# Kernel optimization log

Hardware: AMD Instinct MI355X
Metric: run time of the kernel (lower is better)

## Reference

```python
import jax, jax.numpy as jnp
import numpy as np

N = 102400   # total nodes
F = 400      # node features
E = 1638400  # edges
H = 64       # hidden channels
L = 3        # num_layers (hidden convs); +1 final conv to width 1
K = 300      # sort-pool k
NPER = 400   # nodes per graph (uniform graphs)
B = N // NPER
D = H * L + 1  # total_latent_dim = 193


def setup_inputs() -> dict:
    key = jax.random.key(0)
    ks = jax.random.split(key, 20)
    def lin(k, i, o):
        return jax.random.normal(k, (i, o), jnp.float32) / np.sqrt(i)
    inp = {
        "x": jax.random.normal(ks[0], (N, F), jnp.float32),
        "edge_index": jax.random.randint(ks[1], (2, E), 0, N, jnp.int64),
        "W1": lin(ks[2], F, H), "b1": jnp.zeros((H,), jnp.float32),
        "W2": lin(ks[3], H, H), "b2": jnp.zeros((H,), jnp.float32),
        "W3": lin(ks[4], H, H), "b3": jnp.zeros((H,), jnp.float32),
        "W4": lin(ks[5], H, 1), "b4": jnp.zeros((1,), jnp.float32),
        "cw1": jax.random.normal(ks[6], (16, 1, D), jnp.float32) / np.sqrt(D),
        "cb1": jnp.zeros((16,), jnp.float32),
        "cw2": jax.random.normal(ks[7], (32, 16, 5), jnp.float32) / np.sqrt(16 * 5),
        "cb2": jnp.zeros((32,), jnp.float32),
        "mw1": lin(ks[8], 4672, 32), "mb1": jnp.zeros((32,), jnp.float32),
        "mw2": lin(ks[9], 32, 2), "mb2": jnp.zeros((2,), jnp.float32),
    }
    return inp


def _gcn(x, W, b, src, dst, norm):
    h = x @ W                                   # [N, out]
    msg = h[src] * norm[:, None]                # [E', out]
    out = jax.ops.segment_sum(msg, dst, num_segments=N)
    return out + b


def reference(x, edge_index, W1, b1, W2, b2, W3, b3, W4, b4,
              cw1, cb1, cw2, cb2, mw1, mb1, mw2, mb2):
    # GCN normalization with self-loops (D^-1/2 (A+I) D^-1/2)
    loops = jnp.arange(N, dtype=edge_index.dtype)
    src = jnp.concatenate([edge_index[0], loops])
    dst = jnp.concatenate([edge_index[1], loops])
    deg = jax.ops.segment_sum(jnp.ones_like(src, jnp.float32), dst, num_segments=N)
    dis = jax.lax.rsqrt(jnp.maximum(deg, 1.0))
    norm = dis[src] * dis[dst]

    h1 = jnp.tanh(_gcn(x, W1, b1, src, dst, norm))
    h2 = jnp.tanh(_gcn(h1, W2, b2, src, dst, norm))
    h3 = jnp.tanh(_gcn(h2, W3, b3, src, dst, norm))
    h4 = jnp.tanh(_gcn(h3, W4, b4, src, dst, norm))
    feat = jnp.concatenate([h1, h2, h3, h4], axis=-1)  # [N, D]

    # SortAggregation: per-graph sort by last channel (descending), take top-k
    fg = feat.reshape(B, NPER, D)
    order = jnp.argsort(-fg[:, :, -1], axis=1)[:, :K]  # [B, K]
    pooled = jnp.take_along_axis(fg, order[:, :, None], axis=1)  # [B, K, D]
    z = pooled.reshape(B, 1, K * D)

    dn = ("NCH", "OIH", "NCH")
    z = jax.lax.conv_general_dilated(z, cw1, (D,), "VALID", dimension_numbers=dn)
    z = jax.nn.relu(z + cb1[None, :, None])            # [B, 16, K]
    z = jax.lax.reduce_window(z, -jnp.inf, jax.lax.max, (1, 1, 2), (1, 1, 2), "VALID")
    z = jax.lax.conv_general_dilated(z, cw2, (1,), "VALID", dimension_numbers=dn)
    z = jax.nn.relu(z + cb2[None, :, None])            # [B, 32, 146]
    z = z.reshape(B, -1)                               # [B, 4672]
    z = jax.nn.relu(z @ mw1 + mb1)
    return z @ mw2 + mb2                               # [B, 2]
```

## Files before the change

### kernel.cpp

```cpp
#include <hip/hip_runtime.h>
#include <cstdint>
#include <cstddef>

#define Nn 102400
#define Ff 400
#define Ee 1638400
#define Kk 300
#define Bb 256
#define CAP 64

__device__ __forceinline__ float xla_tanhf(float x) {
    const float c = 7.90531110763549805f;
    float xc = fminf(fmaxf(x, -c), c);
    float x2 = __fmul_rn(xc, xc);
    float p = -2.76076847742355e-16f;
    p = __fadd_rn(__fmul_rn(p, x2),  2.00018790482477e-13f);
    p = __fadd_rn(__fmul_rn(p, x2), -8.60467152213735e-11f);
    p = __fadd_rn(__fmul_rn(p, x2),  5.12229709037114e-08f);
    p = __fadd_rn(__fmul_rn(p, x2),  1.48572235717979e-05f);
    p = __fadd_rn(__fmul_rn(p, x2),  6.37261928875436e-04f);
    p = __fadd_rn(__fmul_rn(p, x2),  4.89352455891786e-03f);
    p = __fmul_rn(p, xc);
    float q = 1.19825839466702e-06f;
    q = __fadd_rn(__fmul_rn(q, x2), 1.18534705686654e-04f);
    q = __fadd_rn(__fmul_rn(q, x2), 2.26843463243900e-03f);
    q = __fadd_rn(__fmul_rn(q, x2), 4.89352518554385e-03f);
    float r = __fdiv_rn(p, q);
    return (fabsf(x) < 0.0004f) ? x : r;
}

__global__ void scat_k(const int* __restrict__ ei, int* __restrict__ fill,
                       int* __restrict__ csr) {
    int g = blockIdx.x * 256 + threadIdx.x;
    int2 d2 = *(const int2*)(ei + Ee + 2 * g);
    int e0 = 2 * g, e1 = 2 * g + 1;
    int p0 = atomicAdd(&fill[(size_t)d2.x * 16], 1);
    int p1 = atomicAdd(&fill[(size_t)d2.y * 16], 1);
    if (p0 < CAP) csr[(size_t)d2.x * CAP + p0] = e0;
    if (p1 < CAP) csr[(size_t)d2.y * CAP + p1] = e1;
}

__global__ void dis_k(const int* __restrict__ fill, float* __restrict__ dis,
                      int* __restrict__ degc) {
    int v = blockIdx.x * 256 + threadIdx.x;
    if (v >= Nn) return;
    int d = fill[(size_t)v * 16];
    degc[v] = d;
    dis[v] = 1.0f / sqrtf((float)(d + 1));
}

template <int CH>
__global__ __launch_bounds__(128) void gemm_2w(const float* __restrict__ A,
                                               const float* __restrict__ B,
                                               float* __restrict__ C) {
    constexpr int K = 16 * CH;
    __shared__ __align__(16) float As[16 * 32];
    __shared__ __align__(16) float Bs[16 * 68];
    int tid = threadIdx.x;
    int w = tid >> 6;
    int lane = tid & 63;
    int tx = lane & 15;
    int ty = lane >> 4;
    int base = blockIdx.x * 32;
    int sr = tid >> 2, sq = tid & 3;
    int bk = tid >> 3, bn = (tid & 7) * 8;
    float acc[8][2] = {};
    for (int ch = 0; ch < CH; ++ch) {
        int k0 = ch * 16;
        float4 av = *(const float4*)(A + (size_t)(base + sr) * K + k0 + sq * 4);
        const float* bp = B + (size_t)(k0 + bk) * 64 + bn;
        float4 b0 = *(const float4*)(bp);
        float4 b1 = *(const float4*)(bp + 4);
        __syncthreads();
        As[(sq * 4 + 0) * 32 + sr] = av.x;
        As[(sq * 4 + 1) * 32 + sr] = av.y;
        As[(sq * 4 + 2) * 32 + sr] = av.z;
        As[(sq * 4 + 3) * 32 + sr] = av.w;
        *(float4*)&Bs[bk * 68 + bn]     = b0;
        *(float4*)&Bs[bk * 68 + bn + 4] = b1;
        __syncthreads();
#pragma unroll
        for (int kk = 0; kk < 16; ++kk) {
            float4 f0 = *(const float4*)&As[kk * 32 + ty * 8];
            float4 f1 = *(const float4*)&As[kk * 32 + ty * 8 + 4];
            float2 bb = *(const float2*)&Bs[kk * 68 + w * 32 + tx * 2];
            float av8[8] = {f0.x, f0.y, f0.z, f0.w, f1.x, f1.y, f1.z, f1.w};
#pragma unroll
            for (int r = 0; r < 8; ++r) {
                acc[r][0] = fmaf(av8[r], bb.x, acc[r][0]);
                acc[r][1] = fmaf(av8[r], bb.y, acc[r][1]);
            }
        }
    }
#pragma unroll
    for (int r = 0; r < 8; ++r) {
        float* cp = C + (size_t)(base + ty * 8 + r) * 64 + w * 32 + tx * 2;
        *(float2*)cp = make_float2(acc[r][0], acc[r][1]);
    }
}

template <int CH>
__global__ __launch_bounds__(64) void gemm_w32(const float* __restrict__ A,
                                               const float* __restrict__ B,
                                               float* __restrict__ C) {
    constexpr int K = 16 * CH;
    __shared__ __align__(16) float As[16 * 32];
    __shared__ __align__(16) float Bs[16][68];
    int tid = threadIdx.x;
    int tx = tid & 15;
    int ty = tid >> 4;
    int base = blockIdx.x * 32;
    int sr = tid >> 1, sh = tid & 1;
    int bk = tid >> 2, bn = (tid & 3) * 16;
    float acc[8][4] = {};
    for (int ch = 0; ch < CH; ++ch) {
        int k0 = ch * 16;
        const float* ap = A + (size_t)(base + sr) * K + k0 + sh * 8;
        float4 v0 = *(const float4*)(ap);
        float4 v1 = *(const float4*)(ap + 4);
        float a8[8] = {v0.x, v0.y, v0.z, v0.w, v1.x, v1.y, v1.z, v1.w};
        float4 bv4[4];
        const float* bp = B + (size_t)(k0 + bk) * 64 + bn;
#pragma unroll
        for (int q = 0; q < 4; ++q) bv4[q] = *(const float4*)(bp + q * 4);
        __syncthreads();
#pragma unroll
        for (int q = 0; q < 8; ++q) As[(sh * 8 + q) * 32 + sr] = a8[q];
#pragma unroll
        for (int q = 0; q < 4; ++q) *(float4*)&Bs[bk][bn + q * 4] = bv4[q];
        __syncthreads();
#pragma unroll
        for (int kk = 0; kk < 16; ++kk) {
            float4 f0 = *(const float4*)&As[kk * 32 + ty * 8];
            float4 f1 = *(const float4*)&As[kk * 32 + ty * 8 + 4];
            float av[8] = {f0.x, f0.y, f0.z, f0.w, f1.x, f1.y, f1.z, f1.w};
            float2 b01 = *(const float2*)&Bs[kk][tx * 2];
            float2 b23 = *(const float2*)&Bs[kk][32 + tx * 2];
            float bv[4] = {b01.x, b01.y, b23.x, b23.y};
#pragma unroll
            for (int r = 0; r < 8; ++r)
#pragma unroll
                for (int c = 0; c < 4; ++c) acc[r][c] = fmaf(av[r], bv[c], acc[r][c]);
        }
    }
#pragma unroll
    for (int r = 0; r < 8; ++r) {
        float* cp = C + (size_t)(base + ty * 8 + r) * 64;
        *(float2*)(cp + tx * 2)      = make_float2(acc[r][0], acc[r][1]);
        *(float2*)(cp + 32 + tx * 2) = make_float2(acc[r][2], acc[r][3]);
    }
}

template <int PHASE>
__global__ __launch_bounds__(256, 4) void agg64_k(const float* __restrict__ t,
                                                  const float* __restrict__ bias,
                                                  const float* __restrict__ dis,
                                                  const int* __restrict__ degc,
                                                  const int* __restrict__ ei,
                                                  int* __restrict__ csr,
                                                  float* __restrict__ nrm,
                                                  float* __restrict__ out,
                                                  const float* __restrict__ W4,
                                                  float* __restrict__ t4) {
    __shared__ int   sidx[4][64];
    __shared__ float snr[4][64];
    int lane = threadIdx.x & 63;
    int wv = __builtin_amdgcn_readfirstlane(threadIdx.x >> 6);
    int v = blockIdx.x * 4 + wv;
    int dv = __builtin_amdgcn_readfirstlane(min(degc[v], CAP));
    float dsv = dis[v];
    float tself = t[(size_t)v * 64 + lane];
    float bsl = bias[lane];
    int idxl;
    float nr;
    if (PHASE == 1) {
        int key = (lane < dv) ? csr[(size_t)v * CAP + lane] : 0x7FFFFFFF;
#pragma unroll
        for (int k = 2; k <= 64; k <<= 1) {
#pragma unroll
            for (int j = k >> 1; j; j >>= 1) {
                int other = __shfl_xor(key, j);
                bool up = ((lane & k) == 0);
                bool lower = ((lane & j) == 0);
                key = (lower == up) ? min(key, other) : max(key, other);
            }
        }
        idxl = v;
        if (lane < dv) idxl = ei[key];
        nr = (lane < dv) ? __fmul_rn(dis[idxl], dsv) : 0.0f;
        csr[(size_t)v * CAP + lane] = idxl;
        nrm[(size_t)v * 64 + lane] = nr;
    } else {
        idxl = (lane < dv) ? csr[(size_t)v * CAP + lane] : v;
        nr = nrm[(size_t)v * 64 + lane];
    }
    sidx[wv][lane] = idxl;
    snr[wv][lane] = nr;
    int dvp = (dv + 31) & ~31;
    float acc = 0.0f;
    for (int j = 0; j < dvp; j += 32) {
        float tv[32], nv[32];
#pragma unroll
        for (int q = 0; q < 32; ++q) {
            int u = __builtin_amdgcn_readfirstlane(sidx[wv][j + q]);
            tv[q] = t[(size_t)u * 64 + lane];
        }
#pragma unroll
        for (int q = 0; q < 32; ++q) nv[q] = snr[wv][j + q];
#pragma unroll
        for (int q = 0; q < 32; ++q)
            acc = __fadd_rn(acc, __fmul_rn(tv[q], nv[q]));
    }
    acc = __fadd_rn(acc, __fmul_rn(tself, __fmul_rn(dsv, dsv)));
    float res = xla_tanhf(__fadd_rn(acc, bsl));
    out[(size_t)v * 64 + lane] = res;
    if (W4 != nullptr) {
        float w4l = W4[lane];
        float a4 = 0.0f;
#pragma unroll
        for (int k = 0; k < 64; ++k) {
            float hk = __shfl(res, k);
            float wk = __shfl(w4l, k);
            a4 = fmaf(hk, wk, a4);
        }
        if (lane == 0) t4[v] = a4;
    }
}

__global__ void agg1_k(const float* __restrict__ t4, const float* __restrict__ dis,
                       const int* __restrict__ degc, const int* __restrict__ csr,
                       const float* __restrict__ nrm,
                       const float* __restrict__ b4, float* __restrict__ h4) {
    int v = blockIdx.x * 256 + threadIdx.x;
    if (v >= Nn) return;
    int dv = min(degc[v], CAP);
    float dsv = dis[v];
    const int* row = csr + (size_t)v * CAP;
    const float* nr = nrm + (size_t)v * 64;
    float acc = 0.0f;
    int j = 0;
    for (; j + 16 <= dv; j += 16) {
        int u[16]; float nv[16], tv[16];
#pragma unroll
        for (int q = 0; q < 16; ++q) nv[q] = nr[j + q];
#pragma unroll
        for (int q = 0; q < 16; ++q) u[q] = row[j + q];
#pragma unroll
        for (int q = 0; q < 16; ++q) tv[q] = t4[u[q]];
#pragma unroll
        for (int q = 0; q < 16; ++q)
            acc = __fadd_rn(acc, __fmul_rn(tv[q], nv[q]));
    }
    for (; j + 4 <= dv; j += 4) {
        int u[4]; float nv[4], tv[4];
#pragma unroll
        for (int q = 0; q < 4; ++q) nv[q] = nr[j + q];
#pragma unroll
        for (int q = 0; q < 4; ++q) u[q] = row[j + q];
#pragma unroll
        for (int q = 0; q < 4; ++q) tv[q] = t4[u[q]];
#pragma unroll
        for (int q = 0; q < 4; ++q)
            acc = __fadd_rn(acc, __fmul_rn(tv[q], nv[q]));
    }
    for (; j < dv; ++j)
        acc = __fadd_rn(acc, __fmul_rn(t4[row[j]], nr[j]));
    acc = __fadd_rn(acc, __fmul_rn(t4[v], __fmul_rn(dsv, dsv)));
    h4[v] = xla_tanhf(__fadd_rn(acc, b4[0]));
}

__global__ __launch_bounds__(512) void sort_k(const float* __restrict__ h4,
                                              int* __restrict__ order) {
    __shared__ unsigned int kv[512];
    __shared__ int ki[512];
    int tid = threadIdx.x, g = blockIdx.x;
    unsigned int key = 0xFFFFFFFFu;
    if (tid < 400) {
        unsigned int u = __float_as_uint(h4[g * 400 + tid]);
        u = (u & 0x80000000u) ? ~u : (u | 0x80000000u);
        key = ~u;
    }
    kv[tid] = key; ki[tid] = tid;
    __syncthreads();
    for (int size = 2; size <= 512; size <<= 1) {
        for (int stride = size >> 1; stride > 0; stride >>= 1) {
            int p = tid ^ stride;
            if (p > tid) {
                bool asc = ((tid & size) == 0);
                unsigned int a = kv[tid], b = kv[p];
                int ia = ki[tid], ib = ki[p];
                bool gt = (a > b) || (a == b && ia > ib);
                if (gt == asc) { kv[tid] = b; kv[p] = a; ki[tid] = ib; ki[p] = ia; }
            }
            __syncthreads();
        }
    }
    if (tid < Kk) order[g * Kk + tid] = ki[tid];
}

__global__ __launch_bounds__(128) void conv1_k(const float* __restrict__ h1,
                                               const float* __restrict__ h2,
                                               const float* __restrict__ h3,
                                               const float* __restrict__ h4,
                                               const int* __restrict__ order,
                                               const float* __restrict__ cw1,
                                               const float* __restrict__ cb1,
                                               float* __restrict__ z1) {
    __shared__ double wt[193 * 16];
    int tid = threadIdx.x, b = blockIdx.y;
    for (int i = tid; i < 193 * 16; i += 128) {
        int c = i / 193, d = i % 193;
        wt[d * 16 + c] = (double)cw1[i];
    }
    __syncthreads();
    int kpos = blockIdx.x * 128 + tid;
    if (kpos >= Kk) return;
    int n = b * 400 + order[b * Kk + kpos];
    double acc[16];
#pragma unroll
    for (int c = 0; c < 16; ++c) acc[c] = (double)cb1[c];
    const float* bases[3] = {h1 + (size_t)n * 64, h2 + (size_t)n * 64, h3 + (size_t)n * 64};
    for (int r = 0; r < 3; ++r) {
        const float* p = bases[r];
        for (int d = 0; d < 64; ++d) {
            double xv = (double)p[d];
            const double* wp = &wt[((size_t)r * 64 + d) * 16];
#pragma unroll
            for (int c = 0; c < 16; ++c) acc[c] += xv * wp[c];
        }
    }
    double xl = (double)h4[n];
    {
        const double* wp = &wt[192 * 16];
#pragma unroll
        for (int c = 0; c < 16; ++c) acc[c] += xl * wp[c];
    }
#pragma unroll
    for (int c = 0; c < 16; ++c)
        z1[((size_t)b * 16 + c) * 300 + kpos] = (float)fmax(acc[c], 0.0);
}

__global__ __launch_bounds__(256) void tail_k(const float* __restrict__ z1,
                                              const float* __restrict__ cw2,
                                              const float* __restrict__ cb2,
                                              const float* __restrict__ mw1,
                                              const float* __restrict__ mb1,
                                              const float* __restrict__ mw2,
                                              const float* __restrict__ mb2,
                                              float* __restrict__ out) {
    __shared__ float lz[16 * 150];
    __shared__ float lw[2560];
    __shared__ float lz3[4672];
    __shared__ double red[256];
    __shared__ double s4[32];
    int b = blockIdx.x, tid = threadIdx.x;
    for (int i = tid; i < 2400; i += 256) {
        int bc = i / 150, j = i % 150;
        const float* zp = z1 + ((size_t)b * 16 + bc) * 300 + 2 * j;
        lz[i] = fmaxf(zp[0], zp[1]);
    }
    for (int i = tid; i < 2560; i += 256) lw[i] = cw2[i];
    __syncthreads();
    for (int o = tid; o < 4672; o += 256) {
        int co = o / 146, j = o % 146;
        float acc = cb2[co];
#pragma unroll
        for (int ci = 0; ci < 16; ++ci)
#pragma unroll
            for (int tt = 0; tt < 5; ++tt)
                acc += lz[ci * 150 + j + tt] * lw[co * 80 + ci * 5 + tt];
        lz3[o] = fmaxf(acc, 0.f);
    }
    __syncthreads();
    int o = tid & 31, part = tid >> 5;
    double acc = 0.0;
    for (int i = part * 584; i < (part + 1) * 584; ++i)
        acc += (double)lz3[i] * (double)mw1[(size_t)i * 32 + o];
    red[tid] = acc;
    __syncthreads();
    if (tid < 32) {
        double s = 0.0;
#pragma unroll
        for (int p = 0; p < 8; ++p) s += red[p * 32 + tid];
        s4[tid] = fmax(s + (double)mb1[tid], 0.0);
    }
    __syncthreads();
    if (tid < 2) {
        double s = (double)mb2[tid];
#pragma unroll
        for (int j = 0; j < 32; ++j) s += s4[j] * (double)mw2[j * 2 + tid];
        out[b * 2 + tid] = (float)s;
    }
}

extern "C" void kernel_launch(void* const* d_in, const int* in_sizes, int n_in,
                              void* d_out, int out_size, void* d_ws, size_t ws_size,
                              hipStream_t stream) {
    const float* x   = (const float*)d_in[0];
    const int*   ei  = (const int*)d_in[1];
    const float* W1  = (const float*)d_in[2];  const float* b1  = (const float*)d_in[3];
    const float* W2  = (const float*)d_in[4];  const float* b2  = (const float*)d_in[5];
    const float* W3  = (const float*)d_in[6];  const float* b3  = (const float*)d_in[7];
    const float* W4  = (const float*)d_in[8];  const float* b4  = (const float*)d_in[9];
    const float* cw1 = (const float*)d_in[10]; const float* cb1 = (const float*)d_in[11];
    const float* cw2 = (const float*)d_in[12]; const float* cb2 = (const float*)d_in[13];
    const float* mw1 = (const float*)d_in[14]; const float* mb1 = (const float*)d_in[15];
    const float* mw2 = (const float*)d_in[16]; const float* mb2 = (const float*)d_in[17];
    float* out = (float*)d_out;

    const size_t N64 = (size_t)Nn * 64;
    float* t    = (float*)d_ws;
    float* h1   = t + N64;
    float* h2   = h1 + N64;
    float* h3   = h2 + N64;
    float* t4   = h3 + N64;
    float* h4   = t4 + Nn;
    float* dis  = h4 + Nn;
    int*   degc = (int*)(dis + Nn);
    int*   fill = degc + Nn;
    int*   csr  = fill + (size_t)Nn * 16;
    float* nrm  = (float*)(csr + (size_t)Nn * CAP);
    int*   order = (int*)(nrm + N64);
    float* z1 = (float*)t;

    hipMemsetAsync(fill, 0, sizeof(int) * (size_t)Nn * 16, stream);

    scat_k<<<Ee / 512, 256, 0, stream>>>(ei, fill, csr);
    dis_k<<<Nn / 256, 256, 0, stream>>>(fill, dis, degc);

    gemm_2w<25><<<Nn / 32, 128, 0, stream>>>(x, W1, t);
    agg64_k<1><<<Nn / 4, 256, 0, stream>>>(t, b1, dis, degc, ei, csr, nrm, h1, nullptr, nullptr);
    gemm_w32<4><<<Nn / 32, 64, 0, stream>>>(h1, W2, t);
    agg64_k<0><<<Nn / 4, 256, 0, stream>>>(t, b2, dis, degc, ei, csr, nrm, h2, nullptr, nullptr);
    gemm_w32<4><<<Nn / 32, 64, 0, stream>>>(h2, W3, t);
    agg64_k<0><<<Nn / 4, 256, 0, stream>>>(t, b3, dis, degc, ei, csr, nrm, h3, W4, t4);

    agg1_k<<<Nn / 256, 256, 0, stream>>>(t4, dis, degc, csr, nrm, b4, h4);

    sort_k<<<Bb, 512, 0, stream>>>(h4, order);
    conv1_k<<<dim3(3, Bb), 128, 0, stream>>>(h1, h2, h3, h4, order, cw1, cb1, z1);
    tail_k<<<Bb, 256, 0, stream>>>(z1, cw2, cb2, mw1, mb1, mw2, mb2, out);
}
```

Measured before the change: 936.0 us.

## Fuse next-layer 64x64 GEMM into aggregation epilogue, two nodes per wave

Drops the separate gemm_w32 launches for W2 and W3. Each aggregation kernel now multiplies its tanh output by the next layer's weight matrix, staged in shared memory, and ping-pongs between two workspace buffers. Each wave also handles two nodes, with the first 32 neighbour gathers for both issued before accumulating, to raise memory-level parallelism. This removes a full write and re-read of the hidden features per layer plus two launches. The cost is extra register pressure from the two 32-wide gather arrays and a per-block load of the 16 KB weight matrix.

```diff
diff --git a/kernel.cpp b/kernel.cpp
--- a/kernel.cpp
+++ b/kernel.cpp
@@ -99,59 +99,7 @@
     }
 }
 
-template <int CH>
-__global__ __launch_bounds__(64) void gemm_w32(const float* __restrict__ A,
-                                               const float* __restrict__ B,
-                                               float* __restrict__ C) {
-    constexpr int K = 16 * CH;
-    __shared__ __align__(16) float As[16 * 32];
-    __shared__ __align__(16) float Bs[16][68];
-    int tid = threadIdx.x;
-    int tx = tid & 15;
-    int ty = tid >> 4;
-    int base = blockIdx.x * 32;
-    int sr = tid >> 1, sh = tid & 1;
-    int bk = tid >> 2, bn = (tid & 3) * 16;
-    float acc[8][4] = {};
-    for (int ch = 0; ch < CH; ++ch) {
-        int k0 = ch * 16;
-        const float* ap = A + (size_t)(base + sr) * K + k0 + sh * 8;
-        float4 v0 = *(const float4*)(ap);
-        float4 v1 = *(const float4*)(ap + 4);
-        float a8[8] = {v0.x, v0.y, v0.z, v0.w, v1.x, v1.y, v1.z, v1.w};
-        float4 bv4[4];
-        const float* bp = B + (size_t)(k0 + bk) * 64 + bn;
-#pragma unroll
-        for (int q = 0; q < 4; ++q) bv4[q] = *(const float4*)(bp + q * 4);
-        __syncthreads();
-#pragma unroll
-        for (int q = 0; q < 8; ++q) As[(sh * 8 + q) * 32 + sr] = a8[q];
-#pragma unroll
-        for (int q = 0; q < 4; ++q) *(float4*)&Bs[bk][bn + q * 4] = bv4[q];
-        __syncthreads();
-#pragma unroll
-        for (int kk = 0; kk < 16; ++kk) {
-            float4 f0 = *(const float4*)&As[kk * 32 + ty * 8];
-            float4 f1 = *(const float4*)&As[kk * 32 + ty * 8 + 4];
-            float av[8] = {f0.x, f0.y, f0.z, f0.w, f1.x, f1.y, f1.z, f1.w};
-            float2 b01 = *(const float2*)&Bs[kk][tx * 2];
-            float2 b23 = *(const float2*)&Bs[kk][32 + tx * 2];
-            float bv[4] = {b01.x, b01.y, b23.x, b23.y};
-#pragma unroll
-            for (int r = 0; r < 8; ++r)
-#pragma unroll
-                for (int c = 0; c < 4; ++c) acc[r][c] = fmaf(av[r], bv[c], acc[r][c]);
-        }
-    }
-#pragma unroll
-    for (int r = 0; r < 8; ++r) {
-        float* cp = C + (size_t)(base + ty * 8 + r) * 64;
-        *(float2*)(cp + tx * 2)      = make_float2(acc[r][0], acc[r][1]);
-        *(float2*)(cp + 32 + tx * 2) = make_float2(acc[r][2], acc[r][3]);
-    }
-}
-
-template <int PHASE>
+template <int PHASE, int EPI>
 __global__ __launch_bounds__(256, 4) void agg64_k(const float* __restrict__ t,
                                                   const float* __restrict__ bias,
                                                   const float* __restrict__ dis,
@@ -160,70 +108,124 @@
                                                   int* __restrict__ csr,
                                                   float* __restrict__ nrm,
                                                   float* __restrict__ out,
-                                                  const float* __restrict__ W4,
-                                                  float* __restrict__ t4) {
-    __shared__ int   sidx[4][64];
-    __shared__ float snr[4][64];
-    int lane = threadIdx.x & 63;
-    int wv = __builtin_amdgcn_readfirstlane(threadIdx.x >> 6);
-    int v = blockIdx.x * 4 + wv;
-    int dv = __builtin_amdgcn_readfirstlane(min(degc[v], CAP));
-    float dsv = dis[v];
-    float tself = t[(size_t)v * 64 + lane];
+                                                  const float* __restrict__ W,
+                                                  float* __restrict__ tn) {
+    __shared__ int   sidx[8][64];
+    __shared__ float snr[8][64];
+    __shared__ float sW[EPI == 64 ? 64 * 64 : 1];
+    int tid = threadIdx.x;
+    int lane = tid & 63;
+    int wv = __builtin_amdgcn_readfirstlane(tid >> 6);
+    if (EPI == 64) {
+        for (int i = tid; i < 64 * 64; i += 256) sW[i] = W[i];
+        __syncthreads();
+    }
+    int v0 = blockIdx.x * 8 + wv * 2;
+    int v1 = v0 + 1;
+    int s0 = wv * 2, s1 = s0 + 1;
+
+    auto prep = [&](int v, int slot) -> int {
+        int dv = __builtin_amdgcn_readfirstlane(min(degc[v], CAP));
+        float dsv = dis[v];
+        int idxl; float nr;
+        if (PHASE == 1) {
+            int key = (lane < dv) ? csr[(size_t)v * CAP + lane] : 0x7FFFFFFF;
+#pragma unroll
+            for (int k = 2; k <= 64; k <<= 1) {
+#pragma unroll
+                for (int j = k >> 1; j; j >>= 1) {
+                    int other = __shfl_xor(key, j);
+                    bool up = ((lane & k) == 0);
+                    bool lower = ((lane & j) == 0);
+                    key = (lower == up) ? min(key, other) : max(key, other);
+                }
+            }
+            idxl = v;
+            if (lane < dv) idxl = ei[key];
+            nr = (lane < dv) ? __fmul_rn(dis[idxl], dsv) : 0.0f;
+            csr[(size_t)v * CAP + lane] = idxl;
+            nrm[(size_t)v * 64 + lane] = nr;
+        } else {
+            idxl = (lane < dv) ? csr[(size_t)v * CAP + lane] : v;
+            nr = nrm[(size_t)v * 64 + lane];
+        }
+        sidx[slot][lane] = idxl;
+        snr[slot][lane] = nr;
+        return dv;
+    };
+    int dv0 = prep(v0, s0);
+    int dv1 = prep(v1, s1);
+    float dsv0 = dis[v0], dsv1 = dis[v1];
+    float tself0 = t[(size_t)v0 * 64 + lane];
+    float tself1 = t[(size_t)v1 * 64 + lane];
     float bsl = bias[lane];
-    int idxl;
-    float nr;
-    if (PHASE == 1) {
-        int key = (lane < dv) ? csr[(size_t)v * CAP + lane] : 0x7FFFFFFF;
-#pragma unroll
-        for (int k = 2; k <= 64; k <<= 1) {
-#pragma unroll
-            for (int j = k >> 1; j; j >>= 1) {
-                int other = __shfl_xor(key, j);
-                bool up = ((lane & k) == 0);
-                bool lower = ((lane & j) == 0);
-                key = (lower == up) ? min(key, other) : max(key, other);
-            }
-        }
-        idxl = v;
-        if (lane < dv) idxl = ei[key];
-        nr = (lane < dv) ? __fmul_rn(dis[idxl], dsv) : 0.0f;
-        csr[(size_t)v * CAP + lane] = idxl;
-        nrm[(size_t)v * 64 + lane] = nr;
-    } else {
-        idxl = (lane < dv) ? csr[(size_t)v * CAP + lane] : v;
-        nr = nrm[(size_t)v * 64 + lane];
-    }
-    sidx[wv][lane] = idxl;
-    snr[wv][lane] = nr;
-    int dvp = (dv + 31) & ~31;
-    float acc = 0.0f;
-    for (int j = 0; j < dvp; j += 32) {
-        float tv[32], nv[32];
+
+    float tv0[32], tv1[32];
+#pragma unroll
+    for (int q = 0; q < 32; ++q) {
+        int u = __builtin_amdgcn_readfirstlane(sidx[s0][q]);
+        tv0[q] = t[(size_t)u * 64 + lane];
+    }
+#pragma unroll
+    for (int q = 0; q < 32; ++q) {
+        int u = __builtin_amdgcn_readfirstlane(sidx[s1][q]);
+        tv1[q] = t[(size_t)u * 64 + lane];
+    }
+    float acc0 = 0.0f, acc1 = 0.0f;
+#pragma unroll
+    for (int q = 0; q < 32; ++q) {
+        acc0 = __fadd_rn(acc0, __fmul_rn(tv0[q], snr[s0][q]));
+        acc1 = __fadd_rn(acc1, __fmul_rn(tv1[q], snr[s1][q]));
+    }
+    if (dv0 > 32) {
+        float tw[32];
 #pragma unroll
         for (int q = 0; q < 32; ++q) {
-            int u = __builtin_amdgcn_readfirstlane(sidx[wv][j + q]);
-            tv[q] = t[(size_t)u * 64 + lane];
-        }
-#pragma unroll
-        for (int q = 0; q < 32; ++q) nv[q] = snr[wv][j + q];
+            int u = __builtin_amdgcn_readfirstlane(sidx[s0][32 + q]);
+            tw[q] = t[(size_t)u * 64 + lane];
+        }
 #pragma unroll
         for (int q = 0; q < 32; ++q)
-            acc = __fadd_rn(acc, __fmul_rn(tv[q], nv[q]));
-    }
-    acc = __fadd_rn(acc, __fmul_rn(tself, __fmul_rn(dsv, dsv)));
-    float res = xla_tanhf(__fadd_rn(acc, bsl));
-    out[(size_t)v * 64 + lane] = res;
-    if (W4 != nullptr) {
-        float w4l = W4[lane];
-        float a4 = 0.0f;
+            acc0 = __fadd_rn(acc0, __fmul_rn(tw[q], snr[s0][32 + q]));
+    }
+    if (dv1 > 32) {
+        float tw[32];
+#pragma unroll
+        for (int q = 0; q < 32; ++q) {
+            int u = __builtin_amdgcn_readfirstlane(sidx[s1][32 + q]);
+            tw[q] = t[(size_t)u * 64 + lane];
+        }
+#pragma unroll
+        for (int q = 0; q < 32; ++q)
+            acc1 = __fadd_rn(acc1, __fmul_rn(tw[q], snr[s1][32 + q]));
+    }
+    acc0 = __fadd_rn(acc0, __fmul_rn(tself0, __fmul_rn(dsv0, dsv0)));
+    acc1 = __fadd_rn(acc1, __fmul_rn(tself1, __fmul_rn(dsv1, dsv1)));
+    float res0 = xla_tanhf(__fadd_rn(acc0, bsl));
+    float res1 = xla_tanhf(__fadd_rn(acc1, bsl));
+    out[(size_t)v0 * 64 + lane] = res0;
+    out[(size_t)v1 * 64 + lane] = res1;
+
+    if (EPI == 64) {
+        float a0 = 0.0f, a1 = 0.0f;
 #pragma unroll
         for (int k = 0; k < 64; ++k) {
-            float hk = __shfl(res, k);
+            float wk = sW[k * 64 + lane];
+            a0 = fmaf(__shfl(res0, k), wk, a0);
+            a1 = fmaf(__shfl(res1, k), wk, a1);
+        }
+        tn[(size_t)v0 * 64 + lane] = a0;
+        tn[(size_t)v1 * 64 + lane] = a1;
+    } else if (EPI == 1) {
+        float w4l = W[lane];
+        float a0 = 0.0f, a1 = 0.0f;
+#pragma unroll
+        for (int k = 0; k < 64; ++k) {
             float wk = __shfl(w4l, k);
-            a4 = fmaf(hk, wk, a4);
-        }
-        if (lane == 0) t4[v] = a4;
+            a0 = fmaf(__shfl(res0, k), wk, a0);
+            a1 = fmaf(__shfl(res1, k), wk, a1);
+        }
+        if (lane == 0) { tn[v0] = a0; tn[v1] = a1; }
     }
 }
 
@@ -409,8 +411,9 @@
     float* out = (float*)d_out;
 
     const size_t N64 = (size_t)Nn * 64;
-    float* t    = (float*)d_ws;
-    float* h1   = t + N64;
+    float* tA   = (float*)d_ws;
+    float* tB   = tA + N64;
+    float* h1   = tB + N64;
     float* h2   = h1 + N64;
     float* h3   = h2 + N64;
     float* t4   = h3 + N64;
@@ -421,19 +424,17 @@
     int*   csr  = fill + (size_t)Nn * 16;
     float* nrm  = (float*)(csr + (size_t)Nn * CAP);
     int*   order = (int*)(nrm + N64);
-    float* z1 = (float*)t;
+    float* z1 = tB;
 
     hipMemsetAsync(fill, 0, sizeof(int) * (size_t)Nn * 16, stream);
 
     scat_k<<<Ee / 512, 256, 0, stream>>>(ei, fill, csr);
     dis_k<<<Nn / 256, 256, 0, stream>>>(fill, dis, degc);
 
-    gemm_2w<25><<<Nn / 32, 128, 0, stream>>>(x, W1, t);
-    agg64_k<1><<<Nn / 4, 256, 0, stream>>>(t, b1, dis, degc, ei, csr, nrm, h1, nullptr, nullptr);
-    gemm_w32<4><<<Nn / 32, 64, 0, stream>>>(h1, W2, t);
-    agg64_k<0><<<Nn / 4, 256, 0, stream>>>(t, b2, dis, degc, ei, csr, nrm, h2, nullptr, nullptr);
-    gemm_w32<4><<<Nn / 32, 64, 0, stream>>>(h2, W3, t);
-    agg64_k<0><<<Nn / 4, 256, 0, stream>>>(t, b3, dis, degc, ei, csr, nrm, h3, W4, t4);
+    gemm_2w<25><<<Nn / 32, 128, 0, stream>>>(x, W1, tA);
+    agg64_k<1, 64><<<Nn / 8, 256, 0, stream>>>(tA, b1, dis, degc, ei, csr, nrm, h1, W2, tB);
+    agg64_k<0, 64><<<Nn / 8, 256, 0, stream>>>(tB, b2, dis, degc, ei, csr, nrm, h2, W3, tA);
+    agg64_k<0, 1> <<<Nn / 8, 256, 0, stream>>>(tA, b3, dis, degc, ei, csr, nrm, h3, W4, t4);
 
     agg1_k<<<Nn / 256, 256, 0, stream>>>(t4, dis, degc, csr, nrm, b4, h4);
 
```

Measured after the change: 1.421 ms. 1.52x slower.

## Fuse next-layer 64x64 GEMM into aggregation epilogue, dropping separate GEMM kernels

Applied to the files above, without the earlier changes.

The separate gemm_w32 launches for W2 and W3 are removed. Each agg64_k block now stages the 64x64 weight matrix in shared memory and, after computing tanh(res), multiplies the row by W through lane shuffles to write the next layer's transformed features directly. A second ping-pong buffer is added so the layer reading one buffer does not overwrite it. This saves two kernel launches and one read of the h1 and h2 arrays, but each block reloads 16KB of weights and adds 64 shuffle-FMA steps per node inside the aggregation kernel, which may raise register and LDS pressure.

```diff
diff --git a/kernel.cpp b/kernel.cpp
--- a/kernel.cpp
+++ b/kernel.cpp
@@ -99,59 +99,7 @@
     }
 }
 
-template <int CH>
-__global__ __launch_bounds__(64) void gemm_w32(const float* __restrict__ A,
-                                               const float* __restrict__ B,
-                                               float* __restrict__ C) {
-    constexpr int K = 16 * CH;
-    __shared__ __align__(16) float As[16 * 32];
-    __shared__ __align__(16) float Bs[16][68];
-    int tid = threadIdx.x;
-    int tx = tid & 15;
-    int ty = tid >> 4;
-    int base = blockIdx.x * 32;
-    int sr = tid >> 1, sh = tid & 1;
-    int bk = tid >> 2, bn = (tid & 3) * 16;
-    float acc[8][4] = {};
-    for (int ch = 0; ch < CH; ++ch) {
-        int k0 = ch * 16;
-        const float* ap = A + (size_t)(base + sr) * K + k0 + sh * 8;
-        float4 v0 = *(const float4*)(ap);
-        float4 v1 = *(const float4*)(ap + 4);
-        float a8[8] = {v0.x, v0.y, v0.z, v0.w, v1.x, v1.y, v1.z, v1.w};
-        float4 bv4[4];
-        const float* bp = B + (size_t)(k0 + bk) * 64 + bn;
-#pragma unroll
-        for (int q = 0; q < 4; ++q) bv4[q] = *(const float4*)(bp + q * 4);
-        __syncthreads();
-#pragma unroll
-        for (int q = 0; q < 8; ++q) As[(sh * 8 + q) * 32 + sr] = a8[q];
-#pragma unroll
-        for (int q = 0; q < 4; ++q) *(float4*)&Bs[bk][bn + q * 4] = bv4[q];
-        __syncthreads();
-#pragma unroll
-        for (int kk = 0; kk < 16; ++kk) {
-            float4 f0 = *(const float4*)&As[kk * 32 + ty * 8];
-            float4 f1 = *(const float4*)&As[kk * 32 + ty * 8 + 4];
-            float av[8] = {f0.x, f0.y, f0.z, f0.w, f1.x, f1.y, f1.z, f1.w};
-            float2 b01 = *(const float2*)&Bs[kk][tx * 2];
-            float2 b23 = *(const float2*)&Bs[kk][32 + tx * 2];
-            float bv[4] = {b01.x, b01.y, b23.x, b23.y};
-#pragma unroll
-            for (int r = 0; r < 8; ++r)
-#pragma unroll
-                for (int c = 0; c < 4; ++c) acc[r][c] = fmaf(av[r], bv[c], acc[r][c]);
-        }
-    }
-#pragma unroll
-    for (int r = 0; r < 8; ++r) {
-        float* cp = C + (size_t)(base + ty * 8 + r) * 64;
-        *(float2*)(cp + tx * 2)      = make_float2(acc[r][0], acc[r][1]);
-        *(float2*)(cp + 32 + tx * 2) = make_float2(acc[r][2], acc[r][3]);
-    }
-}
-
-template <int PHASE>
+template <int PHASE, int EPI>
 __global__ __launch_bounds__(256, 4) void agg64_k(const float* __restrict__ t,
                                                   const float* __restrict__ bias,
                                                   const float* __restrict__ dis,
@@ -160,12 +108,18 @@
                                                   int* __restrict__ csr,
                                                   float* __restrict__ nrm,
                                                   float* __restrict__ out,
-                                                  const float* __restrict__ W4,
-                                                  float* __restrict__ t4) {
+                                                  const float* __restrict__ W,
+                                                  float* __restrict__ tn) {
     __shared__ int   sidx[4][64];
     __shared__ float snr[4][64];
-    int lane = threadIdx.x & 63;
-    int wv = __builtin_amdgcn_readfirstlane(threadIdx.x >> 6);
+    __shared__ float sW[EPI == 64 ? 64 * 64 : 1];
+    int tid = threadIdx.x;
+    int lane = tid & 63;
+    int wv = __builtin_amdgcn_readfirstlane(tid >> 6);
+    if (EPI == 64) {
+        for (int i = tid; i < 64 * 64; i += 256) sW[i] = W[i];
+        __syncthreads();
+    }
     int v = blockIdx.x * 4 + wv;
     int dv = __builtin_amdgcn_readfirstlane(min(degc[v], CAP));
     float dsv = dis[v];
@@ -214,16 +168,19 @@
     acc = __fadd_rn(acc, __fmul_rn(tself, __fmul_rn(dsv, dsv)));
     float res = xla_tanhf(__fadd_rn(acc, bsl));
     out[(size_t)v * 64 + lane] = res;
-    if (W4 != nullptr) {
-        float w4l = W4[lane];
-        float a4 = 0.0f;
-#pragma unroll
-        for (int k = 0; k < 64; ++k) {
-            float hk = __shfl(res, k);
-            float wk = __shfl(w4l, k);
-            a4 = fmaf(hk, wk, a4);
-        }
-        if (lane == 0) t4[v] = a4;
+    if (EPI == 64) {
+        float a = 0.0f;
+#pragma unroll
+        for (int k = 0; k < 64; ++k)
+            a = fmaf(__shfl(res, k), sW[k * 64 + lane], a);
+        tn[(size_t)v * 64 + lane] = a;
+    } else if (EPI == 1) {
+        float w4l = W[lane];
+        float a = 0.0f;
+#pragma unroll
+        for (int k = 0; k < 64; ++k)
+            a = fmaf(__shfl(res, k), __shfl(w4l, k), a);
+        if (lane == 0) tn[v] = a;
     }
 }
 
@@ -409,8 +366,9 @@
     float* out = (float*)d_out;
 
     const size_t N64 = (size_t)Nn * 64;
-    float* t    = (float*)d_ws;
-    float* h1   = t + N64;
+    float* tA   = (float*)d_ws;
+    float* tB   = tA + N64;
+    float* h1   = tB + N64;
     float* h2   = h1 + N64;
     float* h3   = h2 + N64;
     float* t4   = h3 + N64;
@@ -421,19 +379,17 @@
     int*   csr  = fill + (size_t)Nn * 16;
     float* nrm  = (float*)(csr + (size_t)Nn * CAP);
     int*   order = (int*)(nrm + N64);
-    float* z1 = (float*)t;
+    float* z1 = tB;
 
     hipMemsetAsync(fill, 0, sizeof(int) * (size_t)Nn * 16, stream);
 
     scat_k<<<Ee / 512, 256, 0, stream>>>(ei, fill, csr);
     dis_k<<<Nn / 256, 256, 0, stream>>>(fill, dis, degc);
 
-    gemm_2w<25><<<Nn / 32, 128, 0, stream>>>(x, W1, t);
-    agg64_k<1><<<Nn / 4, 256, 0, stream>>>(t, b1, dis, degc, ei, csr, nrm, h1, nullptr, nullptr);
-    gemm_w32<4><<<Nn / 32, 64, 0, stream>>>(h1, W2, t);
-    agg64_k<0><<<Nn / 4, 256, 0, stream>>>(t, b2, dis, degc, ei, csr, nrm, h2, nullptr, nullptr);
-    gemm_w32<4><<<Nn / 32, 64, 0, stream>>>(h2, W3, t);
-    agg64_k<0><<<Nn / 4, 256, 0, stream>>>(t, b3, dis, degc, ei, csr, nrm, h3, W4, t4);
+    gemm_2w<25><<<Nn / 32, 128, 0, stream>>>(x, W1, tA);
+    agg64_k<1, 64><<<Nn / 4, 256, 0, stream>>>(tA, b1, dis, degc, ei, csr, nrm, h1, W2, tB);
+    agg64_k<0, 64><<<Nn / 4, 256, 0, stream>>>(tB, b2, dis, degc, ei, csr, nrm, h2, W3, tA);
+    agg64_k<0, 1> <<<Nn / 4, 256, 0, stream>>>(tA, b3, dis, degc, ei, csr, nrm, h3, W4, t4);
 
     agg1_k<<<Nn / 256, 256, 0, stream>>>(t4, dis, degc, csr, nrm, b4, h4);
 
```

Result: slower. 986.1 us (+5.4%).
